# Kernel optimization log

Hardware: AMD Instinct MI355X
Metric: run time of the kernel (lower is better)

Reference implementation:

```python
import jax, jax.numpy as jnp
import numpy as np

B, D, CROSS = 16384, 2048, 3

def setup_inputs() -> dict:
    key = jax.random.key(0)
    k1, k2 = jax.random.split(key)
    x = jax.random.normal(k1, (B, D), dtype=jnp.float32)
    # glorot_normal for (d,1) weight ~ std sqrt(2/(d+1))
    W = jax.random.normal(k2, (CROSS, D), dtype=jnp.float32) * np.sqrt(2.0 / (D + 1)).astype(np.float32)
    b = jnp.zeros((CROSS, D), dtype=jnp.float32)
    return {"x": x, "W": W, "b": b}

def reference(x, W, b):
    # Original: xl <- (x0 @ xl^T) @ w_i + b_i + xl  with x0, xl shaped [B,d,1].
    # (x0 xl^T) w == x0 * (xl . w), a scalar per row — mathematically identical,
    # avoiding the wasted [B,d,d] outer product.
    x0 = x
    xl = x
    for i in range(CROSS):
        s = jnp.einsum('bd,d->b', xl, W[i])          # [B] scalar dot per row
        xl = x0 * s[:, None] + b[i][None, :] + xl     # scale + bias + residual
    return xl
```

## Files before the change

### kernel.cpp

```cpp
#include <hip/hip_runtime.h>


constexpr int D_DIM  = 2048;
constexpr int NTHREADS = 256;
constexpr int CROSS  = 3;

__global__ __launch_bounds__(NTHREADS)
void cross_network_kernel(const float* __restrict__ x,
                          const float* __restrict__ W,
                          const float* __restrict__ bias,
                          float* __restrict__ out) {
    const int row  = blockIdx.x;
    const int t    = threadIdx.x;
    const int lane = t & 63;
    const int wave = t >> 6;

    const float4* xr = reinterpret_cast<const float4*>(x + (size_t)row * D_DIM);
    const float4 x0a = xr[t];
    const float4 x0b = xr[t + NTHREADS];
    float4 xa = x0a;
    float4 xb = x0b;

    __shared__ float sred[CROSS][4];

#pragma unroll
    for (int i = 0; i < CROSS; ++i) {
        const float4* wr = reinterpret_cast<const float4*>(W + i * D_DIM);
        const float4 w0 = wr[t];
        const float4 w1 = wr[t + NTHREADS];

        float p = xa.x * w0.x + xa.y * w0.y + xa.z * w0.z + xa.w * w0.w
                + xb.x * w1.x + xb.y * w1.y + xb.z * w1.z + xb.w * w1.w;

#pragma unroll
        for (int off = 32; off >= 1; off >>= 1)
            p += __shfl_down(p, off, 64);

        if (lane == 0) sred[i][wave] = p;
        __syncthreads();
        const float s = sred[i][0] + sred[i][1] + sred[i][2] + sred[i][3];

        const float4* br = reinterpret_cast<const float4*>(bias + i * D_DIM);
        const float4 b0 = br[t];
        const float4 b1 = br[t + NTHREADS];

        xa.x = fmaf(x0a.x, s, b0.x + xa.x);
        xa.y = fmaf(x0a.y, s, b0.y + xa.y);
        xa.z = fmaf(x0a.z, s, b0.z + xa.z);
        xa.w = fmaf(x0a.w, s, b0.w + xa.w);
        xb.x = fmaf(x0b.x, s, b1.x + xb.x);
        xb.y = fmaf(x0b.y, s, b1.y + xb.y);
        xb.z = fmaf(x0b.z, s, b1.z + xb.z);
        xb.w = fmaf(x0b.w, s, b1.w + xb.w);
    }

    float4* outr = reinterpret_cast<float4*>(out + (size_t)row * D_DIM);
    outr[t]            = xa;
    outr[t + NTHREADS] = xb;
}

extern "C" void kernel_launch(void* const* d_in, const int* in_sizes, int n_in,
                              void* d_out, int out_size, void* d_ws, size_t ws_size,
                              hipStream_t stream) {
    const float* x    = (const float*)d_in[0];
    const float* W    = (const float*)d_in[1];
    const float* bias = (const float*)d_in[2];
    float* out = (float*)d_out;

    const int B = in_sizes[0] / D_DIM;
    cross_network_kernel<<<B, NTHREADS, 0, stream>>>(x, W, bias, out);
}
```

Measured before the change: 47.87 us.

## Assign one row per wavefront and reduce with wave shuffles only

Each 64-lane wavefront now handles a whole row, holding 8 float4 chunks per lane in registers. The per-row dot product is reduced with butterfly xor shuffles, which removes the shared-memory reduction and the block-wide barrier for each cross layer. Blocks now cover four rows, so the grid shrinks by four. In exchange each lane uses more registers, and the launch-bounds hint asks for four blocks per CU, which may limit occupancy or cause spills. The added B/4 assumption requires B to be a multiple of 4.

```diff
diff --git a/kernel.cpp b/kernel.cpp
--- a/kernel.cpp
+++ b/kernel.cpp
@@ -1,62 +1,60 @@
 #include <hip/hip_runtime.h>
 
 
-constexpr int D_DIM  = 2048;
+constexpr int D_DIM    = 2048;
 constexpr int NTHREADS = 256;
-constexpr int CROSS  = 3;
+constexpr int CROSS    = 3;
+constexpr int CHUNKS   = 8;
 
-__global__ __launch_bounds__(NTHREADS)
+__global__ __launch_bounds__(NTHREADS, 4)
 void cross_network_kernel(const float* __restrict__ x,
                           const float* __restrict__ W,
                           const float* __restrict__ bias,
                           float* __restrict__ out) {
-    const int row  = blockIdx.x;
-    const int t    = threadIdx.x;
-    const int lane = t & 63;
-    const int wave = t >> 6;
+    const int wave = threadIdx.x >> 6;
+    const int lane = threadIdx.x & 63;
+    const int row  = blockIdx.x * 4 + wave;
 
     const float4* xr = reinterpret_cast<const float4*>(x + (size_t)row * D_DIM);
-    const float4 x0a = xr[t];
-    const float4 x0b = xr[t + NTHREADS];
-    float4 xa = x0a;
-    float4 xb = x0b;
 
-    __shared__ float sred[CROSS][4];
+    float4 x0[CHUNKS], xl[CHUNKS];
+#pragma unroll
+    for (int k = 0; k < CHUNKS; ++k) {
+        x0[k] = xr[lane + 64 * k];
+        xl[k] = x0[k];
+    }
 
 #pragma unroll
     for (int i = 0; i < CROSS; ++i) {
         const float4* wr = reinterpret_cast<const float4*>(W + i * D_DIM);
-        const float4 w0 = wr[t];
-        const float4 w1 = wr[t + NTHREADS];
-
-        float p = xa.x * w0.x + xa.y * w0.y + xa.z * w0.z + xa.w * w0.w
-                + xb.x * w1.x + xb.y * w1.y + xb.z * w1.z + xb.w * w1.w;
-
+        float p = 0.0f;
 #pragma unroll
-        for (int off = 32; off >= 1; off >>= 1)
-            p += __shfl_down(p, off, 64);
-
-        if (lane == 0) sred[i][wave] = p;
-        __syncthreads();
-        const float s = sred[i][0] + sred[i][1] + sred[i][2] + sred[i][3];
+        for (int k = 0; k < CHUNKS; ++k) {
+            const float4 w = wr[lane + 64 * k];
+            p = fmaf(xl[k].x, w.x, p);
+            p = fmaf(xl[k].y, w.y, p);
+            p = fmaf(xl[k].z, w.z, p);
+            p = fmaf(xl[k].w, w.w, p);
+        }
+#pragma unroll
+        for (int off = 1; off < 64; off <<= 1)
+            p += __shfl_xor(p, off, 64);
 
         const float4* br = reinterpret_cast<const float4*>(bias + i * D_DIM);
-        const float4 b0 = br[t];
-        const float4 b1 = br[t + NTHREADS];
-
-        xa.x = fmaf(x0a.x, s, b0.x + xa.x);
-        xa.y = fmaf(x0a.y, s, b0.y + xa.y);
-        xa.z = fmaf(x0a.z, s, b0.z + xa.z);
-        xa.w = fmaf(x0a.w, s, b0.w + xa.w);
-        xb.x = fmaf(x0b.x, s, b1.x + xb.x);
-        xb.y = fmaf(x0b.y, s, b1.y + xb.y);
-        xb.z = fmaf(x0b.z, s, b1.z + xb.z);
-        xb.w = fmaf(x0b.w, s, b1.w + xb.w);
+#pragma unroll
+        for (int k = 0; k < CHUNKS; ++k) {
+            const float4 b = br[lane + 64 * k];
+            xl[k].x = fmaf(x0[k].x, p, b.x + xl[k].x);
+            xl[k].y = fmaf(x0[k].y, p, b.y + xl[k].y);
+            xl[k].z = fmaf(x0[k].z, p, b.z + xl[k].z);
+            xl[k].w = fmaf(x0[k].w, p, b.w + xl[k].w);
+        }
     }
 
     float4* outr = reinterpret_cast<float4*>(out + (size_t)row * D_DIM);
-    outr[t]            = xa;
-    outr[t + NTHREADS] = xb;
+#pragma unroll
+    for (int k = 0; k < CHUNKS; ++k)
+        outr[lane + 64 * k] = xl[k];
 }
 
 extern "C" void kernel_launch(void* const* d_in, const int* in_sizes, int n_in,
@@ -68,5 +66,6 @@
     float* out = (float*)d_out;
 
     const int B = in_sizes[0] / D_DIM;
-    cross_network_kernel<<<B, NTHREADS, 0, stream>>>(x, W, bias, out);
+    const int blocks = B / 4;
+    cross_network_kernel<<<blocks, NTHREADS, 0, stream>>>(x, W, bias, out);
 }
```

After: 55.53 us. +16.0%, slower.

## Collapse three cross layers into one fused reduction with closed-form scale

Applied to the files above, without the earlier changes.

Rewrites the recurrence algebraically so the final output is x0*scale + sum of biases, where scale depends on dot products of x0 and the bias partial sums with each W row. All five dot products are computed up front and reduced together with one shared-memory barrier, replacing three sequential reduce-and-sync rounds. The kernel is memory bound (read x, write out), so the gain is limited to lower latency per block. The reassociated sums change float rounding slightly, and the extra bias-times-W reductions add a little compute.

```diff
diff --git a/kernel.cpp b/kernel.cpp
--- a/kernel.cpp
+++ b/kernel.cpp
@@ -1,9 +1,8 @@
 #include <hip/hip_runtime.h>
 
 
-constexpr int D_DIM  = 2048;
+constexpr int D_DIM    = 2048;
 constexpr int NTHREADS = 256;
-constexpr int CROSS  = 3;
 
 __global__ __launch_bounds__(NTHREADS)
 void cross_network_kernel(const float* __restrict__ x,
@@ -16,47 +15,88 @@
     const int wave = t >> 6;
 
     const float4* xr = reinterpret_cast<const float4*>(x + (size_t)row * D_DIM);
-    const float4 x0a = xr[t];
-    const float4 x0b = xr[t + NTHREADS];
-    float4 xa = x0a;
-    float4 xb = x0b;
+    const float4 xa = xr[t];
+    const float4 xb = xr[t + NTHREADS];
 
-    __shared__ float sred[CROSS][4];
+    const float4* w0r = reinterpret_cast<const float4*>(W);
+    const float4* w1r = reinterpret_cast<const float4*>(W + D_DIM);
+    const float4* w2r = reinterpret_cast<const float4*>(W + 2 * D_DIM);
+    const float4* b0r = reinterpret_cast<const float4*>(bias);
+    const float4* b1r = reinterpret_cast<const float4*>(bias + D_DIM);
+    const float4* b2r = reinterpret_cast<const float4*>(bias + 2 * D_DIM);
+
+    const float4 b0a = b0r[t], b0b = b0r[t + NTHREADS];
+    const float4 b1a = b1r[t], b1b = b1r[t + NTHREADS];
+
+    float p0, p1, p2, q1, q2;
+    {
+        const float4 w0a = w0r[t], w0b = w0r[t + NTHREADS];
+        p0 = xa.x*w0a.x + xa.y*w0a.y + xa.z*w0a.z + xa.w*w0a.w
+           + xb.x*w0b.x + xb.y*w0b.y + xb.z*w0b.z + xb.w*w0b.w;
+    }
+    {
+        const float4 w1a = w1r[t], w1b = w1r[t + NTHREADS];
+        p1 = xa.x*w1a.x + xa.y*w1a.y + xa.z*w1a.z + xa.w*w1a.w
+           + xb.x*w1b.x + xb.y*w1b.y + xb.z*w1b.z + xb.w*w1b.w;
+        q1 = b0a.x*w1a.x + b0a.y*w1a.y + b0a.z*w1a.z + b0a.w*w1a.w
+           + b0b.x*w1b.x + b0b.y*w1b.y + b0b.z*w1b.z + b0b.w*w1b.w;
+    }
+    {
+        const float4 w2a = w2r[t], w2b = w2r[t + NTHREADS];
+        p2 = xa.x*w2a.x + xa.y*w2a.y + xa.z*w2a.z + xa.w*w2a.w
+           + xb.x*w2b.x + xb.y*w2b.y + xb.z*w2b.z + xb.w*w2b.w;
+        q2 = (b0a.x+b1a.x)*w2a.x + (b0a.y+b1a.y)*w2a.y
+           + (b0a.z+b1a.z)*w2a.z + (b0a.w+b1a.w)*w2a.w
+           + (b0b.x+b1b.x)*w2b.x + (b0b.y+b1b.y)*w2b.y
+           + (b0b.z+b1b.z)*w2b.z + (b0b.w+b1b.w)*w2b.w;
+    }
 
 #pragma unroll
-    for (int i = 0; i < CROSS; ++i) {
-        const float4* wr = reinterpret_cast<const float4*>(W + i * D_DIM);
-        const float4 w0 = wr[t];
-        const float4 w1 = wr[t + NTHREADS];
-
-        float p = xa.x * w0.x + xa.y * w0.y + xa.z * w0.z + xa.w * w0.w
-                + xb.x * w1.x + xb.y * w1.y + xb.z * w1.z + xb.w * w1.w;
-
-#pragma unroll
-        for (int off = 32; off >= 1; off >>= 1)
-            p += __shfl_down(p, off, 64);
-
-        if (lane == 0) sred[i][wave] = p;
-        __syncthreads();
-        const float s = sred[i][0] + sred[i][1] + sred[i][2] + sred[i][3];
-
-        const float4* br = reinterpret_cast<const float4*>(bias + i * D_DIM);
-        const float4 b0 = br[t];
-        const float4 b1 = br[t + NTHREADS];
-
-        xa.x = fmaf(x0a.x, s, b0.x + xa.x);
-        xa.y = fmaf(x0a.y, s, b0.y + xa.y);
-        xa.z = fmaf(x0a.z, s, b0.z + xa.z);
-        xa.w = fmaf(x0a.w, s, b0.w + xa.w);
-        xb.x = fmaf(x0b.x, s, b1.x + xb.x);
-        xb.y = fmaf(x0b.y, s, b1.y + xb.y);
-        xb.z = fmaf(x0b.z, s, b1.z + xb.z);
-        xb.w = fmaf(x0b.w, s, b1.w + xb.w);
+    for (int off = 32; off >= 1; off >>= 1) {
+        p0 += __shfl_down(p0, off, 64);
+        p1 += __shfl_down(p1, off, 64);
+        p2 += __shfl_down(p2, off, 64);
+        q1 += __shfl_down(q1, off, 64);
+        q2 += __shfl_down(q2, off, 64);
     }
 
+    __shared__ float sred[5][4];
+    if (lane == 0) {
+        sred[0][wave] = p0;
+        sred[1][wave] = p1;
+        sred[2][wave] = p2;
+        sred[3][wave] = q1;
+        sred[4][wave] = q2;
+    }
+    __syncthreads();
+
+    const float d0  = sred[0][0] + sred[0][1] + sred[0][2] + sred[0][3];
+    const float d1  = sred[1][0] + sred[1][1] + sred[1][2] + sred[1][3];
+    const float d2  = sred[2][0] + sred[2][1] + sred[2][2] + sred[2][3];
+    const float c01 = sred[3][0] + sred[3][1] + sred[3][2] + sred[3][3];
+    const float c02 = sred[4][0] + sred[4][1] + sred[4][2] + sred[4][3];
+
+    const float s0 = d0;
+    const float t1 = 1.0f + s0;
+    const float s1 = fmaf(t1, d1, c01);
+    const float t2 = t1 + s1;
+    const float s2 = fmaf(t2, d2, c02);
+    const float scale = t2 + s2;
+
+    const float4 b2a = b2r[t], b2b = b2r[t + NTHREADS];
+    float4 oa, ob;
+    oa.x = fmaf(xa.x, scale, b0a.x + b1a.x + b2a.x);
+    oa.y = fmaf(xa.y, scale, b0a.y + b1a.y + b2a.y);
+    oa.z = fmaf(xa.z, scale, b0a.z + b1a.z + b2a.z);
+    oa.w = fmaf(xa.w, scale, b0a.w + b1a.w + b2a.w);
+    ob.x = fmaf(xb.x, scale, b0b.x + b1b.x + b2b.x);
+    ob.y = fmaf(xb.y, scale, b0b.y + b1b.y + b2b.y);
+    ob.z = fmaf(xb.z, scale, b0b.z + b1b.z + b2b.z);
+    ob.w = fmaf(xb.w, scale, b0b.w + b1b.w + b2b.w);
+
     float4* outr = reinterpret_cast<float4*>(out + (size_t)row * D_DIM);
-    outr[t]            = xa;
-    outr[t + NTHREADS] = xb;
+    outr[t]            = oa;
+    outr[t + NTHREADS] = ob;
 }
 
 extern "C" void kernel_launch(void* const* d_in, const int* in_sizes, int n_in,
```

Result: slower. 49.57 us (+3.5%).

## Collapse cross layers into one closed-form scale and process two rows per block

Applied to the files above, without the earlier changes.

Uses the fact that each layer's output is x0 times a scalar plus a summed bias. All three dot products (x·W_i and the bias·W terms) are computed up front from x0, then reduced together with a single barrier instead of three serial reduce-and-sync rounds. Each block now handles two rows, so the W and bias loads are reused across both. Reordering the floating-point operations changes rounding slightly, and skipping the odd last row assumes B is even.

```diff
diff --git a/kernel.cpp b/kernel.cpp
--- a/kernel.cpp
+++ b/kernel.cpp
@@ -1,62 +1,121 @@
 #include <hip/hip_runtime.h>
 
 
-constexpr int D_DIM  = 2048;
+constexpr int D_DIM    = 2048;
 constexpr int NTHREADS = 256;
-constexpr int CROSS  = 3;
+constexpr int ROWS     = 2;
+
+__device__ __forceinline__ float dot8(const float4 a0, const float4 a1,
+                                      const float4 b0, const float4 b1) {
+    return a0.x*b0.x + a0.y*b0.y + a0.z*b0.z + a0.w*b0.w
+         + a1.x*b1.x + a1.y*b1.y + a1.z*b1.z + a1.w*b1.w;
+}
 
 __global__ __launch_bounds__(NTHREADS)
 void cross_network_kernel(const float* __restrict__ x,
                           const float* __restrict__ W,
                           const float* __restrict__ bias,
                           float* __restrict__ out) {
-    const int row  = blockIdx.x;
+    const int row0 = blockIdx.x * ROWS;
     const int t    = threadIdx.x;
     const int lane = t & 63;
     const int wave = t >> 6;
 
-    const float4* xr = reinterpret_cast<const float4*>(x + (size_t)row * D_DIM);
-    const float4 x0a = xr[t];
-    const float4 x0b = xr[t + NTHREADS];
-    float4 xa = x0a;
-    float4 xb = x0b;
+    const float4* xr0 = reinterpret_cast<const float4*>(x + (size_t)row0 * D_DIM);
+    const float4* xr1 = reinterpret_cast<const float4*>(x + (size_t)(row0 + 1) * D_DIM);
+    const float4 x0a = xr0[t], x0b = xr0[t + NTHREADS];
+    const float4 x1a = xr1[t], x1b = xr1[t + NTHREADS];
 
-    __shared__ float sred[CROSS][4];
+    const float4* w0r = reinterpret_cast<const float4*>(W);
+    const float4* w1r = reinterpret_cast<const float4*>(W + D_DIM);
+    const float4* w2r = reinterpret_cast<const float4*>(W + 2 * D_DIM);
+    const float4* b0r = reinterpret_cast<const float4*>(bias);
+    const float4* b1r = reinterpret_cast<const float4*>(bias + D_DIM);
+    const float4* b2r = reinterpret_cast<const float4*>(bias + 2 * D_DIM);
+
+    float p00, p01, p10, p11, p20, p21, q1, q2;
+    float4 bsa, bsb;
+    {
+        const float4 wa = w0r[t], wb = w0r[t + NTHREADS];
+        p00 = dot8(x0a, x0b, wa, wb);
+        p01 = dot8(x1a, x1b, wa, wb);
+    }
+    {
+        const float4 wa = w1r[t], wb = w1r[t + NTHREADS];
+        p10 = dot8(x0a, x0b, wa, wb);
+        p11 = dot8(x1a, x1b, wa, wb);
+        bsa = b0r[t]; bsb = b0r[t + NTHREADS];
+        q1  = dot8(bsa, bsb, wa, wb);
+    }
+    {
+        const float4 wa = w2r[t], wb = w2r[t + NTHREADS];
+        p20 = dot8(x0a, x0b, wa, wb);
+        p21 = dot8(x1a, x1b, wa, wb);
+        const float4 b1a = b1r[t], b1b = b1r[t + NTHREADS];
+        bsa.x += b1a.x; bsa.y += b1a.y; bsa.z += b1a.z; bsa.w += b1a.w;
+        bsb.x += b1b.x; bsb.y += b1b.y; bsb.z += b1b.z; bsb.w += b1b.w;
+        q2  = dot8(bsa, bsb, wa, wb);
+    }
 
 #pragma unroll
-    for (int i = 0; i < CROSS; ++i) {
-        const float4* wr = reinterpret_cast<const float4*>(W + i * D_DIM);
-        const float4 w0 = wr[t];
-        const float4 w1 = wr[t + NTHREADS];
-
-        float p = xa.x * w0.x + xa.y * w0.y + xa.z * w0.z + xa.w * w0.w
-                + xb.x * w1.x + xb.y * w1.y + xb.z * w1.z + xb.w * w1.w;
-
-#pragma unroll
-        for (int off = 32; off >= 1; off >>= 1)
-            p += __shfl_down(p, off, 64);
-
-        if (lane == 0) sred[i][wave] = p;
-        __syncthreads();
-        const float s = sred[i][0] + sred[i][1] + sred[i][2] + sred[i][3];
-
-        const float4* br = reinterpret_cast<const float4*>(bias + i * D_DIM);
-        const float4 b0 = br[t];
-        const float4 b1 = br[t + NTHREADS];
-
-        xa.x = fmaf(x0a.x, s, b0.x + xa.x);
-        xa.y = fmaf(x0a.y, s, b0.y + xa.y);
-        xa.z = fmaf(x0a.z, s, b0.z + xa.z);
-        xa.w = fmaf(x0a.w, s, b0.w + xa.w);
-        xb.x = fmaf(x0b.x, s, b1.x + xb.x);
-        xb.y = fmaf(x0b.y, s, b1.y + xb.y);
-        xb.z = fmaf(x0b.z, s, b1.z + xb.z);
-        xb.w = fmaf(x0b.w, s, b1.w + xb.w);
+    for (int off = 32; off >= 1; off >>= 1) {
+        p00 += __shfl_down(p00, off, 64);
+        p01 += __shfl_down(p01, off, 64);
+        p10 += __shfl_down(p10, off, 64);
+        p11 += __shfl_down(p11, off, 64);
+        p20 += __shfl_down(p20, off, 64);
+        p21 += __shfl_down(p21, off, 64);
+        q1  += __shfl_down(q1,  off, 64);
+        q2  += __shfl_down(q2,  off, 64);
     }
 
-    float4* outr = reinterpret_cast<float4*>(out + (size_t)row * D_DIM);
-    outr[t]            = xa;
-    outr[t + NTHREADS] = xb;
+    __shared__ float sred[8][4];
+    if (lane == 0) {
+        sred[0][wave] = p00; sred[1][wave] = p01;
+        sred[2][wave] = p10; sred[3][wave] = p11;
+        sred[4][wave] = p20; sred[5][wave] = p21;
+        sred[6][wave] = q1;  sred[7][wave] = q2;
+    }
+    __syncthreads();
+
+    float d[8];
+#pragma unroll
+    for (int k = 0; k < 8; ++k)
+        d[k] = sred[k][0] + sred[k][1] + sred[k][2] + sred[k][3];
+    const float c01 = d[6], c02 = d[7];
+
+    float scale[ROWS];
+#pragma unroll
+    for (int r = 0; r < ROWS; ++r) {
+        const float s0 = d[0 + r];
+        const float t1 = 1.0f + s0;
+        const float s1 = fmaf(t1, d[2 + r], c01);
+        const float t2 = t1 + s1;
+        const float s2 = fmaf(t2, d[4 + r], c02);
+        scale[r] = t2 + s2;
+    }
+
+    {
+        const float4 b2a = b2r[t], b2b = b2r[t + NTHREADS];
+        bsa.x += b2a.x; bsa.y += b2a.y; bsa.z += b2a.z; bsa.w += b2a.w;
+        bsb.x += b2b.x; bsb.y += b2b.y; bsb.z += b2b.z; bsb.w += b2b.w;
+    }
+
+    float4* o0 = reinterpret_cast<float4*>(out + (size_t)row0 * D_DIM);
+    float4* o1 = reinterpret_cast<float4*>(out + (size_t)(row0 + 1) * D_DIM);
+    float4 v;
+    v.x = fmaf(x0a.x, scale[0], bsa.x); v.y = fmaf(x0a.y, scale[0], bsa.y);
+    v.z = fmaf(x0a.z, scale[0], bsa.z); v.w = fmaf(x0a.w, scale[0], bsa.w);
+    o0[t] = v;
+    v.x = fmaf(x0b.x, scale[0], bsb.x); v.y = fmaf(x0b.y, scale[0], bsb.y);
+    v.z = fmaf(x0b.z, scale[0], bsb.z); v.w = fmaf(x0b.w, scale[0], bsb.w);
+    o0[t + NTHREADS] = v;
+    v.x = fmaf(x1a.x, scale[1], bsa.x); v.y = fmaf(x1a.y, scale[1], bsa.y);
+    v.z = fmaf(x1a.z, scale[1], bsa.z); v.w = fmaf(x1a.w, scale[1], bsa.w);
+    o1[t] = v;
+    v.x = fmaf(x1b.x, scale[1], bsb.x); v.y = fmaf(x1b.y, scale[1], bsb.y);
+    v.z = fmaf(x1b.z, scale[1], bsb.z); v.w = fmaf(x1b.w, scale[1], bsb.w);
+    o1[t + NTHREADS] = v;
 }
 
 extern "C" void kernel_launch(void* const* d_in, const int* in_sizes, int n_in,
@@ -68,5 +127,5 @@
     float* out = (float*)d_out;
 
     const int B = in_sizes[0] / D_DIM;
-    cross_network_kernel<<<B, NTHREADS, 0, stream>>>(x, W, bias, out);
+    cross_network_kernel<<<B / ROWS, NTHREADS, 0, stream>>>(x, W, bias, out);
 }
```

Measured after the change: 43.56 us, median of 2. 1.1x faster.
